# Optimization experiments

Hardware: AMD Instinct MI355X
Metric: run time of the kernel (lower is better)

The kernel has to match this reference:

```python
import jax, jax.numpy as jnp
import numpy as np

K = 3  # number of nearest neighbors for interpolation
BIG = 1e10  # masks out cross-batch pairs in the distance matrix


def setup_inputs() -> dict:
    key = jax.random.key(0)
    ks = jax.random.split(key, 8)
    N, Ns, C, Cs, B = 4096, 16384, 256, 128, 4
    Din, H = C + Cs, 256
    return {
        "x": jax.random.normal(ks[0], (N, C), dtype=jnp.float32),
        "pos": jax.random.normal(ks[1], (N, 3), dtype=jnp.float32),
        "batch": jnp.sort(jax.random.randint(ks[2], (N,), 0, B)),
        "x_skip": jax.random.normal(ks[3], (Ns, Cs), dtype=jnp.float32),
        "pos_skip": jax.random.normal(ks[4], (Ns, 3), dtype=jnp.float32),
        "batch_skip": jnp.sort(jax.random.randint(ks[5], (Ns,), 0, B)),
        "W1": jax.random.normal(ks[6], (Din, H), dtype=jnp.float32) * (1.0 / np.sqrt(Din)),
        "b1": jnp.zeros((H,), dtype=jnp.float32),
        "W2": jax.random.normal(ks[7], (H, H), dtype=jnp.float32) * (1.0 / np.sqrt(H)),
        "b2": jnp.zeros((H,), dtype=jnp.float32),
    }


def reference(x, pos, batch, x_skip, pos_skip, batch_skip, W1, b1, W2, b2):
    # knn_interpolate: squared distances from each fine point to all coarse points,
    # masked so neighbors only come from the same batch element.
    d2 = jnp.sum((pos_skip[:, None, :] - pos[None, :, :]) ** 2, axis=-1)  # [Ns, N]
    d2 = jnp.where(batch_skip[:, None] != batch[None, :], BIG, d2)
    neg_d2, idx = jax.lax.top_k(-d2, K)          # k smallest distances, [Ns, K]
    w = 1.0 / jnp.clip(-neg_d2, 1e-16)           # inverse-squared-distance weights
    num = jnp.sum(x[idx] * w[..., None], axis=1)  # [Ns, C] weighted gather-reduce
    y = num / jnp.sum(w, axis=1, keepdims=True)
    # concat skip features, then MLP (Linear-ReLU-Linear-ReLU)
    y = jnp.concatenate([y, x_skip], axis=1)      # [Ns, C + Cs]
    h = jax.nn.relu(y @ W1 + b1)
    out = jax.nn.relu(h @ W2 + b2)
    return (out, pos_skip, batch_skip)
```

## Files before the change

### kernel.cpp

```cpp
#include <hip/hip_runtime.h>
#include <stdint.h>

#define NPTS   4096
#define NSKIP  16384
#define CCH    256
#define CSK    128
#define DIN    384
#define HDIM   256
#define BIGF   1e10f

typedef unsigned short u16;
typedef __attribute__((ext_vector_type(8))) short short8;
typedef __attribute__((ext_vector_type(4))) float floatx4;

__device__ __forceinline__ u16 f2bf(float f) {
    union { float f; uint32_t u; } c; c.f = f;
    uint32_t u = c.u;
    return (u16)((u + 0x7FFFu + ((u >> 16) & 1u)) >> 16);
}

__device__ __forceinline__ double pkkey(float d, int j) {
    return __hiloint2double(__float_as_int(d), j);
}

__global__ __launch_bounds__(256) void prep_knn_kernel(
    const float* __restrict__ W1, const float* __restrict__ W2,
    u16* __restrict__ W1p, u16* __restrict__ W2p,
    const float* __restrict__ pos, const int* __restrict__ batch,
    const float* __restrict__ pos_skip, const int* __restrict__ batch_skip,
    int* __restrict__ idx3, float* __restrict__ w3)
{
    const int bid = blockIdx.x;
    const int t = threadIdx.x;

    if (bid < 80) {
        const float* W = (bid < 48) ? W1 : W2;
        u16* Wp       = (bid < 48) ? W1p : W2p;
        const int KT  = (bid < 48) ? 12 : 8;
        const int g   = ((bid < 48) ? bid : (bid - 48)) * 256 + t;

        const int lane = g & 63;
        const int kt = (g >> 6) % KT;
        const int nt = (g >> 6) / KT;
        const int kbase = kt * 32 + (lane >> 4) * 8;
        const int n = nt * 16 + (lane & 15);
        u16 v[8];
#pragma unroll
        for (int j = 0; j < 8; ++j) v[j] = f2bf(W[(size_t)(kbase + j) * HDIM + n]);
#pragma unroll
        for (int j = 0; j < 8; ++j) Wp[(size_t)g * 8 + j] = v[j];
        return;
    }

    __shared__ int sRange[5];
    if (t < 5) {
        int lo = 0, hi = NPTS;
        while (lo < hi) {
            const int m = (lo + hi) >> 1;
            if (batch[m] < t) lo = m + 1; else hi = m;
        }
        sRange[t] = lo;
    }
    __syncthreads();

    const int i = (bid - 80) * 8 + (t >> 5);
    const int sub = t & 31;
    const int b = batch_skip[i];
    const int start = sRange[b], end = sRange[b + 1];

    const float px = pos_skip[i * 3 + 0];
    const float py = pos_skip[i * 3 + 1];
    const float pz = pos_skip[i * 3 + 2];

    const double BIGKEY = pkkey(BIGF, 0x7FFFFFFF);
    double k0 = BIGKEY, k1 = BIGKEY, k2 = BIGKEY;

    for (int j = start + sub; j < end; j += 32) {
        const float qx = pos[j * 3 + 0];
        const float qy = pos[j * 3 + 1];
        const float qz = pos[j * 3 + 2];
        const float dx = __fsub_rn(px, qx);
        const float dy = __fsub_rn(py, qy);
        const float dz = __fsub_rn(pz, qz);
        const float dd = __fadd_rn(__fadd_rn(__fmul_rn(dx, dx), __fmul_rn(dy, dy)),
                                   __fmul_rn(dz, dz));
        const double kk = pkkey(dd, j);
        const double u0 = fmax(k0, kk); k0 = fmin(k0, kk);
        const double u1 = fmax(k1, u0); k1 = fmin(k1, u0);
        k2 = fmin(k2, u1);
    }

#pragma unroll
    for (int m = 1; m < 32; m <<= 1) {
        const double o0 = __shfl_xor(k0, m);
        const double o1 = __shfl_xor(k1, m);
        const double o2 = __shfl_xor(k2, m);
        double u0 = fmax(k0, o0); k0 = fmin(k0, o0);
        double u1 = fmax(k1, u0); k1 = fmin(k1, u0);
        k2 = fmin(k2, u1);
        u1 = fmax(k1, o1); k1 = fmin(k1, o1);
        k2 = fmin(k2, u1);
        k2 = fmin(k2, o2);
    }

    if (sub == 0) {
        const float d0 = __int_as_float(__double2hiint(k0));
        const float d1 = __int_as_float(__double2hiint(k1));
        const float d2 = __int_as_float(__double2hiint(k2));
        const float w0 = 1.0f / fmaxf(d0, 1e-16f);
        const float w1 = 1.0f / fmaxf(d1, 1e-16f);
        const float w2 = 1.0f / fmaxf(d2, 1e-16f);
        const float inv = 1.0f / (w0 + w1 + w2);
        idx3[i * 3 + 0] = __double2loint(k0);
        idx3[i * 3 + 1] = __double2loint(k1);
        idx3[i * 3 + 2] = __double2loint(k2);
        w3[i * 3 + 0] = w0 * inv; w3[i * 3 + 1] = w1 * inv; w3[i * 3 + 2] = w2 * inv;
    }
}

__global__ __launch_bounds__(1024, 8) void fused_mlp_kernel(
    const float* __restrict__ x, const float* __restrict__ x_skip,
    const int* __restrict__ idx3, const float* __restrict__ w3,
    const u16* __restrict__ W1p, const float* __restrict__ b1,
    const u16* __restrict__ W2p, const float* __restrict__ b2,
    const float* __restrict__ pos_skip, const int* __restrict__ batch_skip,
    float* __restrict__ out)
{
    __shared__ u16 sA[32 * 392];
    __shared__ float sOut[32 * 256];
    const int t = threadIdx.x;
    const int row0 = blockIdx.x * 32;
    const int wave = t >> 6, lane = t & 63;
    const int quad = lane >> 4, ml = lane & 15;

#pragma unroll
    for (int k = 0; k < 2; ++k) {
        const int g = t + 1024 * k;
        const int row = g >> 6, c4 = g & 63;
        const int R = row0 + row;
        const int i0 = idx3[R * 3 + 0], i1 = idx3[R * 3 + 1], i2 = idx3[R * 3 + 2];
        const float w0 = w3[R * 3 + 0], w1 = w3[R * 3 + 1], w2 = w3[R * 3 + 2];
        const float4 v0 = *(const float4*)(x + (size_t)i0 * CCH + c4 * 4);
        const float4 v1 = *(const float4*)(x + (size_t)i1 * CCH + c4 * 4);
        const float4 v2 = *(const float4*)(x + (size_t)i2 * CCH + c4 * 4);
        const float a  = w0 * v0.x + w1 * v1.x + w2 * v2.x;
        const float bq = w0 * v0.y + w1 * v1.y + w2 * v2.y;
        const float cq = w0 * v0.z + w1 * v1.z + w2 * v2.z;
        const float dq = w0 * v0.w + w1 * v1.w + w2 * v2.w;
        uint2 pk;
        pk.x = (uint32_t)f2bf(a)  | ((uint32_t)f2bf(bq) << 16);
        pk.y = (uint32_t)f2bf(cq) | ((uint32_t)f2bf(dq) << 16);
        *(uint2*)(sA + row * 392 + c4 * 4) = pk;
    }
    {
        const int row = t >> 5, c4 = t & 31;
        const float4 v = *(const float4*)(x_skip + (size_t)(row0 + row) * CSK + c4 * 4);
        uint2 pk;
        pk.x = (uint32_t)f2bf(v.x) | ((uint32_t)f2bf(v.y) << 16);
        pk.y = (uint32_t)f2bf(v.z) | ((uint32_t)f2bf(v.w) << 16);
        *(uint2*)(sA + row * 392 + CCH + c4 * 4) = pk;
    }
    __syncthreads();

    floatx4 acc[2] = {};
    {
        const u16* aA = sA + ml * 392 + quad * 8;
        for (int kt = 0; kt < 12; ++kt) {
            short8 a0 = *(const short8*)(aA + kt * 32);
            short8 a1 = *(const short8*)(aA + 16 * 392 + kt * 32);
            short8 bfr = *(const short8*)(W1p + (size_t)((wave * 12 + kt) * 64 + lane) * 8);
            acc[0] = __builtin_amdgcn_mfma_f32_16x16x32_bf16(a0, bfr, acc[0], 0, 0, 0);
            acc[1] = __builtin_amdgcn_mfma_f32_16x16x32_bf16(a1, bfr, acc[1], 0, 0, 0);
        }
    }
    __syncthreads();

    {
        const int n = wave * 16 + ml;
        const float bv = b1[n];
#pragma unroll
        for (int mt = 0; mt < 2; ++mt) {
#pragma unroll
            for (int r = 0; r < 4; ++r) {
                const int m = mt * 16 + quad * 4 + r;
                sA[m * 264 + n] = f2bf(fmaxf(acc[mt][r] + bv, 0.0f));
            }
        }
    }
    __syncthreads();

    floatx4 acc2[2] = {};
    {
        const u16* aH = sA + ml * 264 + quad * 8;
        for (int kt = 0; kt < 8; ++kt) {
            short8 a0 = *(const short8*)(aH + kt * 32);
            short8 a1 = *(const short8*)(aH + 16 * 264 + kt * 32);
            short8 bfr = *(const short8*)(W2p + (size_t)((wave * 8 + kt) * 64 + lane) * 8);
            acc2[0] = __builtin_amdgcn_mfma_f32_16x16x32_bf16(a0, bfr, acc2[0], 0, 0, 0);
            acc2[1] = __builtin_amdgcn_mfma_f32_16x16x32_bf16(a1, bfr, acc2[1], 0, 0, 0);
        }
    }

    {
        const int n = wave * 16 + ml;
        const float bv = b2[n];
#pragma unroll
        for (int mt = 0; mt < 2; ++mt) {
#pragma unroll
            for (int r = 0; r < 4; ++r) {
                const int m = mt * 16 + quad * 4 + r;
                sOut[m * 256 + n] = fmaxf(acc2[mt][r] + bv, 0.0f);
            }
        }
    }
    __syncthreads();
    {
        float* dst = out + (size_t)row0 * HDIM;
#pragma unroll
        for (int k = 0; k < 2; ++k) {
            const int e = t + 1024 * k;
            *(float4*)(dst + e * 4) = *(const float4*)(sOut + e * 4);
        }
    }

    if (t < 128) {
        const int e = blockIdx.x * 128 + t;
        const size_t base = (size_t)NSKIP * HDIM;
        if (e < NSKIP * 3) out[base + e] = pos_skip[e];
        else               out[base + e] = (float)batch_skip[e - NSKIP * 3];
    }
}

extern "C" void kernel_launch(void* const* d_in, const int* in_sizes, int n_in,
                              void* d_out, int out_size, void* d_ws, size_t ws_size,
                              hipStream_t stream) {
    const float* x         = (const float*)d_in[0];
    const float* pos       = (const float*)d_in[1];
    const int*   batch     = (const int*)d_in[2];
    const float* x_skip    = (const float*)d_in[3];
    const float* pos_skip  = (const float*)d_in[4];
    const int*   batch_skip= (const int*)d_in[5];
    const float* W1        = (const float*)d_in[6];
    const float* b1        = (const float*)d_in[7];
    const float* W2        = (const float*)d_in[8];
    const float* b2        = (const float*)d_in[9];
    float* out = (float*)d_out;

    char* ws = (char*)d_ws;
    u16*    W1p   = (u16*)ws;
    u16*    W2p   = (u16*)(ws + 196608);
    int*    idx3  = (int*)(ws + 327680);
    float*  w3    = (float*)(ws + 524288);

    prep_knn_kernel<<<80 + NSKIP / 8, 256, 0, stream>>>(W1, W2, W1p, W2p,
                                                        pos, batch,
                                                        pos_skip, batch_skip,
                                                        idx3, w3);
    fused_mlp_kernel<<<NSKIP / 32, 1024, 0, stream>>>(x, x_skip, idx3, w3,
                                                      W1p, b1, W2p, b2,
                                                      pos_skip, batch_skip, out);
}
```

Baseline: 114.3 us.

## Push first linear layer before interpolation gather using linearity

Uses the linearity of the weighted neighbor sum: it projects the 4096 coarse features through the first 256 columns of W1 once (Z = x·W1a) and the skip features through the rest (S = x_skip·W1b) in a new kernel. The fused kernel then gathers three 256-wide rows of Z, blends them with the interpolation weights, adds S and the bias, and applies ReLU before the second GEMM. This cuts first-layer GEMM work on the gathered side from 16384 rows to 4096. The cost is an extra launch and fp32 Z/S buffers in workspace that have to be written and read back. Rounding also changes, since the interpolation now runs after a bf16 GEMM.

```diff
diff --git a/kernel.cpp b/kernel.cpp
--- a/kernel.cpp
+++ b/kernel.cpp
@@ -118,75 +118,143 @@
     }
 }
 
+__global__ __launch_bounds__(512) void zs_kernel(
+    const float* __restrict__ x, const float* __restrict__ x_skip,
+    const u16* __restrict__ W1p,
+    float* __restrict__ Zb, float* __restrict__ Sb)
+{
+    __shared__ u16 sA[32 * 264];
+    __shared__ float sOut[32 * 256];
+    const int t = threadIdx.x;
+    const int wave = t >> 6, lane = t & 63;
+    const int quad = lane >> 4, ml = lane & 15;
+    const bool isZ = blockIdx.x < 128;
+    const int brow = (isZ ? blockIdx.x : blockIdx.x - 128) * 32;
+
+    if (isZ) {
+#pragma unroll
+        for (int k = 0; k < 4; ++k) {
+            const int g = t + 512 * k;
+            const int row = g >> 6, c4 = g & 63;
+            const float4 v = *(const float4*)(x + (size_t)(brow + row) * CCH + c4 * 4);
+            uint2 pk;
+            pk.x = (uint32_t)f2bf(v.x) | ((uint32_t)f2bf(v.y) << 16);
+            pk.y = (uint32_t)f2bf(v.z) | ((uint32_t)f2bf(v.w) << 16);
+            *(uint2*)(sA + row * 264 + c4 * 4) = pk;
+        }
+    } else {
+#pragma unroll
+        for (int k = 0; k < 2; ++k) {
+            const int g = t + 512 * k;
+            const int row = g >> 5, c4 = g & 31;
+            const float4 v = *(const float4*)(x_skip + (size_t)(brow + row) * CSK + c4 * 4);
+            uint2 pk;
+            pk.x = (uint32_t)f2bf(v.x) | ((uint32_t)f2bf(v.y) << 16);
+            pk.y = (uint32_t)f2bf(v.z) | ((uint32_t)f2bf(v.w) << 16);
+            *(uint2*)(sA + row * 136 + c4 * 4) = pk;
+        }
+    }
+    __syncthreads();
+
+    floatx4 acc[2][2] = {};
+    if (isZ) {
+        const u16* aA = sA + ml * 264 + quad * 8;
+        for (int kt = 0; kt < 8; ++kt) {
+            short8 a0 = *(const short8*)(aA + kt * 32);
+            short8 a1 = *(const short8*)(aA + 16 * 264 + kt * 32);
+#pragma unroll
+            for (int nt = 0; nt < 2; ++nt) {
+                const int ntile = wave * 2 + nt;
+                short8 bfr = *(const short8*)(W1p + (size_t)((ntile * 12 + kt) * 64 + lane) * 8);
+                acc[0][nt] = __builtin_amdgcn_mfma_f32_16x16x32_bf16(a0, bfr, acc[0][nt], 0, 0, 0);
+                acc[1][nt] = __builtin_amdgcn_mfma_f32_16x16x32_bf16(a1, bfr, acc[1][nt], 0, 0, 0);
+            }
+        }
+    } else {
+        const u16* aA = sA + ml * 136 + quad * 8;
+        for (int kt = 0; kt < 4; ++kt) {
+            short8 a0 = *(const short8*)(aA + kt * 32);
+            short8 a1 = *(const short8*)(aA + 16 * 136 + kt * 32);
+#pragma unroll
+            for (int nt = 0; nt < 2; ++nt) {
+                const int ntile = wave * 2 + nt;
+                short8 bfr = *(const short8*)(W1p + (size_t)((ntile * 12 + 8 + kt) * 64 + lane) * 8);
+                acc[0][nt] = __builtin_amdgcn_mfma_f32_16x16x32_bf16(a0, bfr, acc[0][nt], 0, 0, 0);
+                acc[1][nt] = __builtin_amdgcn_mfma_f32_16x16x32_bf16(a1, bfr, acc[1][nt], 0, 0, 0);
+            }
+        }
+    }
+
+#pragma unroll
+    for (int mt = 0; mt < 2; ++mt) {
+#pragma unroll
+        for (int nt = 0; nt < 2; ++nt) {
+            const int n = (wave * 2 + nt) * 16 + ml;
+#pragma unroll
+            for (int r = 0; r < 4; ++r) {
+                const int m = mt * 16 + quad * 4 + r;
+                sOut[m * 256 + n] = acc[mt][nt][r];
+            }
+        }
+    }
+    __syncthreads();
+    {
+        float* dst = (isZ ? Zb : Sb) + (size_t)brow * 256;
+#pragma unroll
+        for (int k = 0; k < 4; ++k) {
+            const int e = t + 512 * k;
+            *(float4*)(dst + e * 4) = *(const float4*)(sOut + e * 4);
+        }
+    }
+}
+
 __global__ __launch_bounds__(1024, 8) void fused_mlp_kernel(
-    const float* __restrict__ x, const float* __restrict__ x_skip,
+    const float* __restrict__ Zb, const float* __restrict__ Sb,
     const int* __restrict__ idx3, const float* __restrict__ w3,
-    const u16* __restrict__ W1p, const float* __restrict__ b1,
-    const u16* __restrict__ W2p, const float* __restrict__ b2,
+    const u16* __restrict__ W2p, const float* __restrict__ b1,
+    const float* __restrict__ b2,
     const float* __restrict__ pos_skip, const int* __restrict__ batch_skip,
     float* __restrict__ out)
 {
-    __shared__ u16 sA[32 * 392];
+    __shared__ u16 sA[32 * 264];
     __shared__ float sOut[32 * 256];
     const int t = threadIdx.x;
     const int row0 = blockIdx.x * 32;
     const int wave = t >> 6, lane = t & 63;
     const int quad = lane >> 4, ml = lane & 15;
-
-#pragma unroll
-    for (int k = 0; k < 2; ++k) {
-        const int g = t + 1024 * k;
-        const int row = g >> 6, c4 = g & 63;
-        const int R = row0 + row;
-        const int i0 = idx3[R * 3 + 0], i1 = idx3[R * 3 + 1], i2 = idx3[R * 3 + 2];
-        const float w0 = w3[R * 3 + 0], w1 = w3[R * 3 + 1], w2 = w3[R * 3 + 2];
-        const float4 v0 = *(const float4*)(x + (size_t)i0 * CCH + c4 * 4);
-        const float4 v1 = *(const float4*)(x + (size_t)i1 * CCH + c4 * 4);
-        const float4 v2 = *(const float4*)(x + (size_t)i2 * CCH + c4 * 4);
-        const float a  = w0 * v0.x + w1 * v1.x + w2 * v2.x;
-        const float bq = w0 * v0.y + w1 * v1.y + w2 * v2.y;
-        const float cq = w0 * v0.z + w1 * v1.z + w2 * v2.z;
-        const float dq = w0 * v0.w + w1 * v1.w + w2 * v2.w;
-        uint2 pk;
-        pk.x = (uint32_t)f2bf(a)  | ((uint32_t)f2bf(bq) << 16);
-        pk.y = (uint32_t)f2bf(cq) | ((uint32_t)f2bf(dq) << 16);
-        *(uint2*)(sA + row * 392 + c4 * 4) = pk;
-    }
-    {
-        const int row = t >> 5, c4 = t & 31;
-        const float4 v = *(const float4*)(x_skip + (size_t)(row0 + row) * CSK + c4 * 4);
-        uint2 pk;
-        pk.x = (uint32_t)f2bf(v.x) | ((uint32_t)f2bf(v.y) << 16);
-        pk.y = (uint32_t)f2bf(v.z) | ((uint32_t)f2bf(v.w) << 16);
-        *(uint2*)(sA + row * 392 + CCH + c4 * 4) = pk;
-    }
-    __syncthreads();
-
-    floatx4 acc[2] = {};
-    {
-        const u16* aA = sA + ml * 392 + quad * 8;
-        for (int kt = 0; kt < 12; ++kt) {
-            short8 a0 = *(const short8*)(aA + kt * 32);
-            short8 a1 = *(const short8*)(aA + 16 * 392 + kt * 32);
-            short8 bfr = *(const short8*)(W1p + (size_t)((wave * 12 + kt) * 64 + lane) * 8);
-            acc[0] = __builtin_amdgcn_mfma_f32_16x16x32_bf16(a0, bfr, acc[0], 0, 0, 0);
-            acc[1] = __builtin_amdgcn_mfma_f32_16x16x32_bf16(a1, bfr, acc[1], 0, 0, 0);
-        }
-    }
-    __syncthreads();
-
-    {
-        const int n = wave * 16 + ml;
-        const float bv = b1[n];
-#pragma unroll
-        for (int mt = 0; mt < 2; ++mt) {
-#pragma unroll
-            for (int r = 0; r < 4; ++r) {
-                const int m = mt * 16 + quad * 4 + r;
-                sA[m * 264 + n] = f2bf(fmaxf(acc[mt][r] + bv, 0.0f));
-            }
-        }
-    }
+    const int rl = t >> 5, c8 = t & 31;
+
+    const float* Sp = Sb + (size_t)(row0 + rl) * 256 + c8 * 8;
+    const float4 s0 = *(const float4*)Sp;
+    const float4 s1 = *(const float4*)(Sp + 4);
+
+    const int R = row0 + rl;
+    const int i0 = idx3[R * 3 + 0], i1 = idx3[R * 3 + 1], i2 = idx3[R * 3 + 2];
+    const float w0 = w3[R * 3 + 0], w1 = w3[R * 3 + 1], w2 = w3[R * 3 + 2];
+    const float4 z00 = *(const float4*)(Zb + (size_t)i0 * 256 + c8 * 8);
+    const float4 z01 = *(const float4*)(Zb + (size_t)i0 * 256 + c8 * 8 + 4);
+    const float4 z10 = *(const float4*)(Zb + (size_t)i1 * 256 + c8 * 8);
+    const float4 z11 = *(const float4*)(Zb + (size_t)i1 * 256 + c8 * 8 + 4);
+    const float4 z20 = *(const float4*)(Zb + (size_t)i2 * 256 + c8 * 8);
+    const float4 z21 = *(const float4*)(Zb + (size_t)i2 * 256 + c8 * 8 + 4);
+    const float4 bb0 = *(const float4*)(b1 + c8 * 8);
+    const float4 bb1 = *(const float4*)(b1 + c8 * 8 + 4);
+
+    float h[8];
+    h[0] = w0 * z00.x + w1 * z10.x + w2 * z20.x + s0.x + bb0.x;
+    h[1] = w0 * z00.y + w1 * z10.y + w2 * z20.y + s0.y + bb0.y;
+    h[2] = w0 * z00.z + w1 * z10.z + w2 * z20.z + s0.z + bb0.z;
+    h[3] = w0 * z00.w + w1 * z10.w + w2 * z20.w + s0.w + bb0.w;
+    h[4] = w0 * z01.x + w1 * z11.x + w2 * z21.x + s1.x + bb1.x;
+    h[5] = w0 * z01.y + w1 * z11.y + w2 * z21.y + s1.y + bb1.y;
+    h[6] = w0 * z01.z + w1 * z11.z + w2 * z21.z + s1.z + bb1.z;
+    h[7] = w0 * z01.w + w1 * z11.w + w2 * z21.w + s1.w + bb1.w;
+    uint4 pk;
+    pk.x = (uint32_t)f2bf(fmaxf(h[0], 0.0f)) | ((uint32_t)f2bf(fmaxf(h[1], 0.0f)) << 16);
+    pk.y = (uint32_t)f2bf(fmaxf(h[2], 0.0f)) | ((uint32_t)f2bf(fmaxf(h[3], 0.0f)) << 16);
+    pk.z = (uint32_t)f2bf(fmaxf(h[4], 0.0f)) | ((uint32_t)f2bf(fmaxf(h[5], 0.0f)) << 16);
+    pk.w = (uint32_t)f2bf(fmaxf(h[6], 0.0f)) | ((uint32_t)f2bf(fmaxf(h[7], 0.0f)) << 16);
+    *(uint4*)(sA + rl * 264 + c8 * 8) = pk;
     __syncthreads();
 
     floatx4 acc2[2] = {};
@@ -251,12 +319,15 @@
     u16*    W2p   = (u16*)(ws + 196608);
     int*    idx3  = (int*)(ws + 327680);
     float*  w3    = (float*)(ws + 524288);
+    float*  Zb    = (float*)(ws + 720896);
+    float*  Sb    = (float*)(ws + 4915200);
 
     prep_knn_kernel<<<80 + NSKIP / 8, 256, 0, stream>>>(W1, W2, W1p, W2p,
                                                         pos, batch,
                                                         pos_skip, batch_skip,
                                                         idx3, w3);
-    fused_mlp_kernel<<<NSKIP / 32, 1024, 0, stream>>>(x, x_skip, idx3, w3,
-                                                      W1p, b1, W2p, b2,
+    zs_kernel<<<128 + NSKIP / 32, 512, 0, stream>>>(x, x_skip, W1p, Zb, Sb);
+    fused_mlp_kernel<<<NSKIP / 32, 1024, 0, stream>>>(Zb, Sb, idx3, w3,
+                                                      W2p, b1, b2,
                                                       pos_skip, batch_skip, out);
 }
```

Result: slower. 119.9 us (+5.0%).

## Fuse kNN search into MLP kernel and pad positions to float4

Applied to the files above, without the earlier changes.

Moves the brute-force 3-nearest-neighbour search out of the prep kernel and into the fused MLP kernel. Each 1024-thread block now computes the neighbours and weights for its own 32 rows and keeps them in shared memory, so the idx3/w3 global round trip goes away. The prep kernel now only converts the weights and writes a float4-padded copy of pos, so the kNN loop can use single vector loads. The cost is a longer per-block serial phase: the search runs before the gather and GEMMs in the same block, and every block repeats the batch-range binary search.

```diff
diff --git a/kernel.cpp b/kernel.cpp
--- a/kernel.cpp
+++ b/kernel.cpp
@@ -23,104 +23,39 @@
     return __hiloint2double(__float_as_int(d), j);
 }
 
-__global__ __launch_bounds__(256) void prep_knn_kernel(
+__global__ __launch_bounds__(256) void prep_kernel(
     const float* __restrict__ W1, const float* __restrict__ W2,
     u16* __restrict__ W1p, u16* __restrict__ W2p,
-    const float* __restrict__ pos, const int* __restrict__ batch,
-    const float* __restrict__ pos_skip, const int* __restrict__ batch_skip,
-    int* __restrict__ idx3, float* __restrict__ w3)
+    const float* __restrict__ pos, float4* __restrict__ pos4)
 {
     const int bid = blockIdx.x;
     const int t = threadIdx.x;
 
-    if (bid < 80) {
-        const float* W = (bid < 48) ? W1 : W2;
-        u16* Wp       = (bid < 48) ? W1p : W2p;
-        const int KT  = (bid < 48) ? 12 : 8;
-        const int g   = ((bid < 48) ? bid : (bid - 48)) * 256 + t;
-
-        const int lane = g & 63;
-        const int kt = (g >> 6) % KT;
-        const int nt = (g >> 6) / KT;
-        const int kbase = kt * 32 + (lane >> 4) * 8;
-        const int n = nt * 16 + (lane & 15);
-        u16 v[8];
-#pragma unroll
-        for (int j = 0; j < 8; ++j) v[j] = f2bf(W[(size_t)(kbase + j) * HDIM + n]);
-#pragma unroll
-        for (int j = 0; j < 8; ++j) Wp[(size_t)g * 8 + j] = v[j];
-        return;
-    }
-
-    __shared__ int sRange[5];
-    if (t < 5) {
-        int lo = 0, hi = NPTS;
-        while (lo < hi) {
-            const int m = (lo + hi) >> 1;
-            if (batch[m] < t) lo = m + 1; else hi = m;
-        }
-        sRange[t] = lo;
-    }
-    __syncthreads();
-
-    const int i = (bid - 80) * 8 + (t >> 5);
-    const int sub = t & 31;
-    const int b = batch_skip[i];
-    const int start = sRange[b], end = sRange[b + 1];
-
-    const float px = pos_skip[i * 3 + 0];
-    const float py = pos_skip[i * 3 + 1];
-    const float pz = pos_skip[i * 3 + 2];
-
-    const double BIGKEY = pkkey(BIGF, 0x7FFFFFFF);
-    double k0 = BIGKEY, k1 = BIGKEY, k2 = BIGKEY;
-
-    for (int j = start + sub; j < end; j += 32) {
-        const float qx = pos[j * 3 + 0];
-        const float qy = pos[j * 3 + 1];
-        const float qz = pos[j * 3 + 2];
-        const float dx = __fsub_rn(px, qx);
-        const float dy = __fsub_rn(py, qy);
-        const float dz = __fsub_rn(pz, qz);
-        const float dd = __fadd_rn(__fadd_rn(__fmul_rn(dx, dx), __fmul_rn(dy, dy)),
-                                   __fmul_rn(dz, dz));
-        const double kk = pkkey(dd, j);
-        const double u0 = fmax(k0, kk); k0 = fmin(k0, kk);
-        const double u1 = fmax(k1, u0); k1 = fmin(k1, u0);
-        k2 = fmin(k2, u1);
-    }
-
-#pragma unroll
-    for (int m = 1; m < 32; m <<= 1) {
-        const double o0 = __shfl_xor(k0, m);
-        const double o1 = __shfl_xor(k1, m);
-        const double o2 = __shfl_xor(k2, m);
-        double u0 = fmax(k0, o0); k0 = fmin(k0, o0);
-        double u1 = fmax(k1, u0); k1 = fmin(k1, u0);
-        k2 = fmin(k2, u1);
-        u1 = fmax(k1, o1); k1 = fmin(k1, o1);
-        k2 = fmin(k2, u1);
-        k2 = fmin(k2, o2);
-    }
-
-    if (sub == 0) {
-        const float d0 = __int_as_float(__double2hiint(k0));
-        const float d1 = __int_as_float(__double2hiint(k1));
-        const float d2 = __int_as_float(__double2hiint(k2));
-        const float w0 = 1.0f / fmaxf(d0, 1e-16f);
-        const float w1 = 1.0f / fmaxf(d1, 1e-16f);
-        const float w2 = 1.0f / fmaxf(d2, 1e-16f);
-        const float inv = 1.0f / (w0 + w1 + w2);
-        idx3[i * 3 + 0] = __double2loint(k0);
-        idx3[i * 3 + 1] = __double2loint(k1);
-        idx3[i * 3 + 2] = __double2loint(k2);
-        w3[i * 3 + 0] = w0 * inv; w3[i * 3 + 1] = w1 * inv; w3[i * 3 + 2] = w2 * inv;
-    }
-}
-
-__global__ __launch_bounds__(1024, 8) void fused_mlp_kernel(
+    const float* W = (bid < 48) ? W1 : W2;
+    u16* Wp       = (bid < 48) ? W1p : W2p;
+    const int KT  = (bid < 48) ? 12 : 8;
+    const int g   = ((bid < 48) ? bid : (bid - 48)) * 256 + t;
+
+    const int lane = g & 63;
+    const int kt = (g >> 6) % KT;
+    const int nt = (g >> 6) / KT;
+    const int kbase = kt * 32 + (lane >> 4) * 8;
+    const int n = nt * 16 + (lane & 15);
+    u16 v[8];
+#pragma unroll
+    for (int j = 0; j < 8; ++j) v[j] = f2bf(W[(size_t)(kbase + j) * HDIM + n]);
+#pragma unroll
+    for (int j = 0; j < 8; ++j) Wp[(size_t)g * 8 + j] = v[j];
+
+    if (bid >= 48 && bid < 64) {
+        const int p = (bid - 48) * 256 + t;
+        pos4[p] = make_float4(pos[p * 3 + 0], pos[p * 3 + 1], pos[p * 3 + 2], 0.0f);
+    }
+}
+
+__global__ __launch_bounds__(1024, 8) void mega_kernel(
     const float* __restrict__ x, const float* __restrict__ x_skip,
-    const int* __restrict__ idx3, const float* __restrict__ w3,
+    const float4* __restrict__ pos4, const int* __restrict__ batch,
     const u16* __restrict__ W1p, const float* __restrict__ b1,
     const u16* __restrict__ W2p, const float* __restrict__ b2,
     const float* __restrict__ pos_skip, const int* __restrict__ batch_skip,
@@ -128,18 +63,96 @@
 {
     __shared__ u16 sA[32 * 392];
     __shared__ float sOut[32 * 256];
+    __shared__ int   sIdx[32 * 3];
+    __shared__ float sWgt[32 * 3];
+    __shared__ int   sRange[5];
     const int t = threadIdx.x;
     const int row0 = blockIdx.x * 32;
     const int wave = t >> 6, lane = t & 63;
     const int quad = lane >> 4, ml = lane & 15;
 
+    if (t < 5) {
+        int lo = 0, hi = NPTS;
+        while (lo < hi) {
+            const int m = (lo + hi) >> 1;
+            if (batch[m] < t) lo = m + 1; else hi = m;
+        }
+        sRange[t] = lo;
+    }
+    {
+        const int row = t >> 5, c4 = t & 31;
+        const float4 v = *(const float4*)(x_skip + (size_t)(row0 + row) * CSK + c4 * 4);
+        uint2 pk;
+        pk.x = (uint32_t)f2bf(v.x) | ((uint32_t)f2bf(v.y) << 16);
+        pk.y = (uint32_t)f2bf(v.z) | ((uint32_t)f2bf(v.w) << 16);
+        *(uint2*)(sA + row * 392 + CCH + c4 * 4) = pk;
+    }
+    __syncthreads();
+
+    {
+        const int rl = t >> 5;
+        const int sub = t & 31;
+        const int i = row0 + rl;
+        const int b = batch_skip[i];
+        const int start = sRange[b], end = sRange[b + 1];
+
+        const float px = pos_skip[i * 3 + 0];
+        const float py = pos_skip[i * 3 + 1];
+        const float pz = pos_skip[i * 3 + 2];
+
+        const double BIGKEY = pkkey(BIGF, 0x7FFFFFFF);
+        double k0 = BIGKEY, k1 = BIGKEY, k2 = BIGKEY;
+
+        for (int j = start + sub; j < end; j += 32) {
+            const float4 q = pos4[j];
+            const float dx = __fsub_rn(px, q.x);
+            const float dy = __fsub_rn(py, q.y);
+            const float dz = __fsub_rn(pz, q.z);
+            const float dd = __fadd_rn(__fadd_rn(__fmul_rn(dx, dx), __fmul_rn(dy, dy)),
+                                       __fmul_rn(dz, dz));
+            const double kk = pkkey(dd, j);
+            const double u0 = fmax(k0, kk); k0 = fmin(k0, kk);
+            const double u1 = fmax(k1, u0); k1 = fmin(k1, u0);
+            k2 = fmin(k2, u1);
+        }
+
+#pragma unroll
+        for (int m = 1; m < 32; m <<= 1) {
+            const double o0 = __shfl_xor(k0, m);
+            const double o1 = __shfl_xor(k1, m);
+            const double o2 = __shfl_xor(k2, m);
+            double u0 = fmax(k0, o0); k0 = fmin(k0, o0);
+            double u1 = fmax(k1, u0); k1 = fmin(k1, u0);
+            k2 = fmin(k2, u1);
+            u1 = fmax(k1, o1); k1 = fmin(k1, o1);
+            k2 = fmin(k2, u1);
+            k2 = fmin(k2, o2);
+        }
+
+        if (sub == 0) {
+            const float d0 = __int_as_float(__double2hiint(k0));
+            const float d1 = __int_as_float(__double2hiint(k1));
+            const float d2 = __int_as_float(__double2hiint(k2));
+            const float w0 = 1.0f / fmaxf(d0, 1e-16f);
+            const float w1 = 1.0f / fmaxf(d1, 1e-16f);
+            const float w2 = 1.0f / fmaxf(d2, 1e-16f);
+            const float inv = 1.0f / (w0 + w1 + w2);
+            sIdx[rl * 3 + 0] = __double2loint(k0);
+            sIdx[rl * 3 + 1] = __double2loint(k1);
+            sIdx[rl * 3 + 2] = __double2loint(k2);
+            sWgt[rl * 3 + 0] = w0 * inv;
+            sWgt[rl * 3 + 1] = w1 * inv;
+            sWgt[rl * 3 + 2] = w2 * inv;
+        }
+    }
+    __syncthreads();
+
 #pragma unroll
     for (int k = 0; k < 2; ++k) {
         const int g = t + 1024 * k;
         const int row = g >> 6, c4 = g & 63;
-        const int R = row0 + row;
-        const int i0 = idx3[R * 3 + 0], i1 = idx3[R * 3 + 1], i2 = idx3[R * 3 + 2];
-        const float w0 = w3[R * 3 + 0], w1 = w3[R * 3 + 1], w2 = w3[R * 3 + 2];
+        const int i0 = sIdx[row * 3 + 0], i1 = sIdx[row * 3 + 1], i2 = sIdx[row * 3 + 2];
+        const float w0 = sWgt[row * 3 + 0], w1 = sWgt[row * 3 + 1], w2 = sWgt[row * 3 + 2];
         const float4 v0 = *(const float4*)(x + (size_t)i0 * CCH + c4 * 4);
         const float4 v1 = *(const float4*)(x + (size_t)i1 * CCH + c4 * 4);
         const float4 v2 = *(const float4*)(x + (size_t)i2 * CCH + c4 * 4);
@@ -151,14 +164,6 @@
         pk.x = (uint32_t)f2bf(a)  | ((uint32_t)f2bf(bq) << 16);
         pk.y = (uint32_t)f2bf(cq) | ((uint32_t)f2bf(dq) << 16);
         *(uint2*)(sA + row * 392 + c4 * 4) = pk;
-    }
-    {
-        const int row = t >> 5, c4 = t & 31;
-        const float4 v = *(const float4*)(x_skip + (size_t)(row0 + row) * CSK + c4 * 4);
-        uint2 pk;
-        pk.x = (uint32_t)f2bf(v.x) | ((uint32_t)f2bf(v.y) << 16);
-        pk.y = (uint32_t)f2bf(v.z) | ((uint32_t)f2bf(v.w) << 16);
-        *(uint2*)(sA + row * 392 + CCH + c4 * 4) = pk;
     }
     __syncthreads();
 
@@ -249,14 +254,10 @@
     char* ws = (char*)d_ws;
     u16*    W1p   = (u16*)ws;
     u16*    W2p   = (u16*)(ws + 196608);
-    int*    idx3  = (int*)(ws + 327680);
-    float*  w3    = (float*)(ws + 524288);
-
-    prep_knn_kernel<<<80 + NSKIP / 8, 256, 0, stream>>>(W1, W2, W1p, W2p,
-                                                        pos, batch,
-                                                        pos_skip, batch_skip,
-                                                        idx3, w3);
-    fused_mlp_kernel<<<NSKIP / 32, 1024, 0, stream>>>(x, x_skip, idx3, w3,
-                                                      W1p, b1, W2p, b2,
-                                                      pos_skip, batch_skip, out);
-}
+    float4* pos4  = (float4*)(ws + 327680);
+
+    prep_kernel<<<80, 256, 0, stream>>>(W1, W2, W1p, W2p, pos, pos4);
+    mega_kernel<<<NSKIP / 32, 1024, 0, stream>>>(x, x_skip, pos4, batch,
+                                                 W1p, b1, W2p, b2,
+                                                 pos_skip, batch_skip, out);
+}
```

Result: faster. 108.7 us, median of 2 (-4.8%).
